# Performance work log

Hardware: AMD Instinct MI355X
Metric: run time of the kernel (lower is better)

Reference implementation:

```python
import jax, jax.numpy as jnp
import numpy as np

B, N, IN_DIM, OUT_DIM, H = 8, 1024, 256, 256, 4
HD = OUT_DIM // H  # head_dim = 64
NEG = -1e9
EPS = 1e-5


def setup_inputs() -> dict:
    key = jax.random.key(0)
    ks = jax.random.split(key, 9)
    h = jax.random.normal(ks[0], (B, N, IN_DIM), dtype=jnp.float32)
    adj = jax.random.randint(ks[1], (N, N), 0, 2, dtype=jnp.int32)
    adj = adj.at[jnp.arange(N), jnp.arange(N)].set(1)  # self loops so no empty rows
    s = 1.0 / np.sqrt(IN_DIM)
    W = jax.random.uniform(ks[2], (H, IN_DIM, HD), jnp.float32, -s, s)
    sa = 1.0 / np.sqrt(2 * HD)
    a1 = jax.random.uniform(ks[3], (H, HD), jnp.float32, -sa, sa)
    a2 = jax.random.uniform(ks[4], (H, HD), jnp.float32, -sa, sa)
    sp = 1.0 / np.sqrt(OUT_DIM)
    proj_w = jax.random.uniform(ks[5], (OUT_DIM, OUT_DIM), jnp.float32, -sp, sp)
    proj_b = jax.random.uniform(ks[6], (OUT_DIM,), jnp.float32, -sp, sp)
    gamma = jnp.ones((OUT_DIM,), jnp.float32)
    beta = jnp.zeros((OUT_DIM,), jnp.float32)
    return {"h": h, "adj": adj, "W": W, "a1": a1, "a2": a2,
            "proj_w": proj_w, "proj_b": proj_b, "gamma": gamma, "beta": beta}


def reference(h, adj, W, a1, a2, proj_w, proj_b, gamma, beta):
    # Wh: [B,H,N,HD]
    Wh = jnp.einsum('bni,hid->bhnd', h, W)
    # Decompose a([Wh_i || Wh_j]) = a1.Wh_i + a2.Wh_j (same math as concat+linear)
    si = jnp.einsum('bhnd,hd->bhn', Wh, a1)  # [B,H,N]
    sj = jnp.einsum('bhnd,hd->bhn', Wh, a2)
    e = jax.nn.leaky_relu(si[:, :, :, None] + sj[:, :, None, :], 0.2)  # [B,H,N,N]
    mask = (adj == 0)  # [N,N]
    e = jnp.where(mask[None, None], NEG, e)
    alpha = jax.nn.softmax(e, axis=-1)
    out = jnp.einsum('bhnm,bhmd->bhnd', alpha, Wh)  # [B,H,N,HD]
    h_multi = out.transpose(0, 2, 1, 3).reshape(B, N, OUT_DIM)  # concat heads
    h_out = jnp.einsum('bnd,od->bno', h_multi, proj_w) + proj_b
    h_out = h_out + h  # residual (in_dim == out_dim)
    mu = jnp.mean(h_out, axis=-1, keepdims=True)
    var = jnp.mean(jnp.square(h_out - mu), axis=-1, keepdims=True)
    return (h_out - mu) * jax.lax.rsqrt(var + EPS) * gamma + beta
```

## Files before the change

### kernel.cpp

```cpp
#include <hip/hip_runtime.h>
#include <hip/hip_bf16.h>

#define NN 1024
#define LOG2E 1.44269504088896f

typedef __attribute__((ext_vector_type(8))) short short8;
typedef __attribute__((ext_vector_type(4))) float floatx4;
typedef __attribute__((ext_vector_type(4))) int intx4;
typedef __attribute__((ext_vector_type(2))) int intx2;

static __device__ __forceinline__ unsigned pk2(float f0, float f1) {
    unsigned u0 = __float_as_uint(f0) + 0x8000u;
    unsigned u1 = __float_as_uint(f1) + 0x8000u;
    return __builtin_amdgcn_perm(u1, u0, 0x07060302u);
}
static __device__ __forceinline__ short8 pk8(floatx4 v0, floatx4 v1) {
    union { intx4 i; short8 s; } u;
    u.i[0] = (int)pk2(v0[0], v0[1]); u.i[1] = (int)pk2(v0[2], v0[3]);
    u.i[2] = (int)pk2(v1[0], v1[1]); u.i[3] = (int)pk2(v1[2], v1[3]);
    return u.s;
}
static __device__ __forceinline__ void load_lds16(const void* gsrc, void* lds) {
    __builtin_amdgcn_global_load_lds(
        (const __attribute__((address_space(1))) void*)gsrc,
        (__attribute__((address_space(3))) void*)lds, 16, 0, 0);
}

__global__ __launch_bounds__(256) void prep_kernel(
    const float* __restrict__ W, const float* __restrict__ proj_w,
    const int* __restrict__ adj,
    __hip_bfloat16* __restrict__ WTb,
    __hip_bfloat16* __restrict__ pwb,
    unsigned* __restrict__ adjT)
{
    int blk = blockIdx.x, t = threadIdx.x;
    if (blk < 16) {
        int o = blk * 16 + (t >> 4);
        int hh = o >> 6, d = o & 63;
        #pragma unroll
        for (int kk = 0; kk < 16; ++kk) {
            int k = (t & 15) + 16 * kk;
            WTb[(size_t)o * 256 + k] = __float2bfloat16(W[((size_t)hh * 256 + k) * 64 + d]);
        }
    } else if (blk < 32) {
        size_t base = (size_t)(blk - 16) * 4096 + (size_t)t * 16;
        #pragma unroll
        for (int k = 0; k < 16; k += 8) {
            floatx4 v0 = *(const floatx4*)(proj_w + base + k);
            floatx4 v1 = *(const floatx4*)(proj_w + base + k + 4);
            *(short8*)(pwb + base + k) = pk8(v0, v1);
        }
    } else {
        int n = (blk - 32) * 8 + (t >> 5);
        int wd = t & 31;
        const int* arow = adj + (size_t)n * NN + wd * 32;
        unsigned bits = 0;
        #pragma unroll
        for (int j4 = 0; j4 < 8; ++j4) {
            intx4 v = *(const intx4*)(arow + j4 * 4);
            #pragma unroll
            for (int j = 0; j < 4; ++j) if (v[j] != 0) bits |= (1u << (j4 * 4 + j));
        }
        adjT[(size_t)wd * NN + n] = bits;
    }
}

__global__ __launch_bounds__(512) void wh_kernel(
    const float* __restrict__ h,
    const __hip_bfloat16* __restrict__ WTb,
    const float* __restrict__ a1, const float* __restrict__ a2,
    __hip_bfloat16* __restrict__ WhTt,
    float* __restrict__ si, float* __restrict__ sj)
{
    __shared__ __align__(16) __hip_bfloat16 WTbs[8][4096];
    __shared__ float redsi[2][4][4][16];
    __shared__ float redsj[2][4][4][16];

    int t = threadIdx.x;
    int w = t >> 6, l = t & 63;
    int rt = w >> 2, ds = w & 3;
    int rl = l & 15, q = l >> 4;
    int bx = blockIdx.x;
    int bb = bx >> 5, tb = bx & 31;

    short8 af[8];
    const float* Arow = h + ((size_t)bb * 1024 + tb * 32 + rt * 16 + rl) * 256 + q * 8;
    #pragma unroll
    for (int k0 = 0; k0 < 8; ++k0) {
        floatx4 v0 = *(const floatx4*)(Arow + k0 * 32);
        floatx4 v1 = *(const floatx4*)(Arow + k0 * 32 + 4);
        af[k0] = pk8(v0, v1);
    }

    int d = ds * 16 + rl;
    int s = rt * 16 + q * 4;
    size_t toff = (size_t)d * 32 + (((s >> 3) ^ (d & 3)) * 8) + (s & 7);
    int srow_ = l >> 5;

    #pragma unroll
    for (int ph = 0; ph < 2; ++ph) {
        if (ph) __syncthreads();
        #pragma unroll
        for (int k = 0; k < 8; ++k) {
            int row = k * 2 + srow_;
            int g = (l & 31) ^ (row & 7);
            load_lds16(WTb + (size_t)(ph * 128 + w * 16 + row) * 256 + g * 8, &WTbs[w][k * 512]);
        }
        __syncthreads();

        #pragma unroll
        for (int jj = 0; jj < 2; ++jj) {
            int head = ph * 2 + jj;
            int lt = ds + 4 * jj;
            floatx4 acc = {0.f, 0.f, 0.f, 0.f};
            #pragma unroll
            for (int k0 = 0; k0 < 8; ++k0) {
                int p = ((k0 << 2) + q) ^ (rl & 7);
                short8 bf = *(const short8*)(&WTbs[lt][rl * 256 + p * 8]);
                acc = __builtin_amdgcn_mfma_f32_16x16x32_bf16(af[k0], bf, acc, 0, 0, 0);
            }

            intx2 pr;
            pr[0] = (int)pk2(acc[0], acc[1]);
            pr[1] = (int)pk2(acc[2], acc[3]);
            *(intx2*)(WhTt + ((size_t)(bb * 4 + head) * 32 + tb) * 2048 + toff) = pr;

            float av1 = a1[head * 64 + d] * LOG2E;
            float av2 = a2[head * 64 + d] * LOG2E;
            #pragma unroll
            for (int i = 0; i < 4; ++i) {
                float p1 = acc[i] * av1, p2 = acc[i] * av2;
                #pragma unroll
                for (int off = 1; off < 16; off <<= 1) {
                    p1 += __shfl_xor(p1, off, 64);
                    p2 += __shfl_xor(p2, off, 64);
                }
                if (rl == 0) { redsi[rt][ds][head][q * 4 + i] = p1; redsj[rt][ds][head][q * 4 + i] = p2; }
            }
        }
    }
    __syncthreads();

    if (t < 128) {
        int head = t >> 5, u = t & 31, rt2 = u >> 4, row = u & 15;
        si[(size_t)(bb * 4 + head) * NN + tb * 32 + rt2 * 16 + row] =
            redsi[rt2][0][head][row] + redsi[rt2][1][head][row] +
            redsi[rt2][2][head][row] + redsi[rt2][3][head][row];
    } else if (t < 256) {
        int u2 = t - 128;
        int head = u2 >> 5, u = u2 & 31, rt2 = u >> 4, row = u & 15;
        sj[(size_t)(bb * 4 + head) * NN + tb * 32 + rt2 * 16 + row] =
            redsj[rt2][0][head][row] + redsj[rt2][1][head][row] +
            redsj[rt2][2][head][row] + redsj[rt2][3][head][row];
    }
}

__global__ __launch_bounds__(256, 4) void attn_kernel(
    const unsigned* __restrict__ adjT,
    const __hip_bfloat16* __restrict__ WhTt,
    const float* __restrict__ si, const float* __restrict__ sj,
    __hip_bfloat16* __restrict__ hmg)
{
    __shared__ __align__(16) __hip_bfloat16 pl[4][16][72];
    __shared__ float accs[4][64][17];
    __shared__ float lsums[4][16];

    int bx = blockIdx.x, t = threadIdx.x;
    int w = t >> 6, l = t & 63;
    int rl = l & 15, q = l >> 4;
    int head = bx & 3, tile = (bx >> 2) & 63, b = bx >> 8;
    int n0 = tile * 16;
    int bh = b * 4 + head;
    int r = l >> 2, cg = l & 3;
    int nr = n0 + r;

    float sii = si[(size_t)bh * NN + nr];
    const float* sjr = sj + (size_t)bh * NN;
    const __hip_bfloat16* Tbh = WhTt + (size_t)bh * 32 * 2048;

    float lsum = 0.f;
    floatx4 acc[4] = { {0,0,0,0}, {0,0,0,0}, {0,0,0,0}, {0,0,0,0} };

    #pragma unroll 2
    for (int it = 0; it < 4; ++it) {
        int mabs = w * 256 + it * 64;
        int t0 = mabs >> 5;
        short8 bf[8];
        #pragma unroll
        for (int ks = 0; ks < 2; ++ks) {
            #pragma unroll
            for (int dt = 0; dt < 4; ++dt)
                bf[ks * 4 + dt] = *(const short8*)(Tbh + (size_t)(t0 + ks) * 2048
                                    + (dt * 16 + rl) * 32 + ((q ^ (rl & 3)) * 8));
        }
        unsigned wA = adjT[(size_t)t0 * NN + nr];
        unsigned wB = adjT[(size_t)(t0 + 1) * NN + nr];
        unsigned half = (cg < 2 ? wA : wB) >> ((cg & 1) * 16);
        int mb = mabs + cg * 16;
        #pragma unroll
        for (int c4 = 0; c4 < 4; ++c4) {
            floatx4 s4 = *(const floatx4*)(sjr + mb + c4 * 4);
            float pv[4];
            #pragma unroll
            for (int k = 0; k < 4; ++k) {
                float x = sii + s4[k];
                x = fmaxf(x, 0.2f * x);
                x = ((half >> (c4 * 4 + k)) & 1u) ? x : -1e9f;
                pv[k] = exp2f(x);
                lsum += pv[k];
            }
            intx2 two;
            two[0] = (int)pk2(pv[0], pv[1]);
            two[1] = (int)pk2(pv[2], pv[3]);
            *(intx2*)(&pl[w][r][cg * 16 + c4 * 4]) = two;
        }
        #pragma unroll
        for (int ks = 0; ks < 2; ++ks) {
            short8 afr = *(const short8*)(&pl[w][rl][ks * 32 + q * 8]);
            #pragma unroll
            for (int dt = 0; dt < 4; ++dt)
                acc[dt] = __builtin_amdgcn_mfma_f32_16x16x32_bf16(afr, bf[ks * 4 + dt], acc[dt], 0, 0, 0);
        }
    }

    lsum += __shfl_xor(lsum, 1, 64);
    lsum += __shfl_xor(lsum, 2, 64);
    if (cg == 0) lsums[w][r] = lsum;
    #pragma unroll
    for (int dt = 0; dt < 4; ++dt) {
        #pragma unroll
        for (int i = 0; i < 4; ++i)
            accs[w][l][dt * 4 + i] = acc[dt][i];
    }
    __syncthreads();

    #pragma unroll
    for (int i = 0; i < 4; ++i) {
        int row = q * 4 + i;
        float riv = 1.f / (lsums[0][row] + lsums[1][row] + lsums[2][row] + lsums[3][row]);
        float cc = accs[0][l][w * 4 + i] + accs[1][l][w * 4 + i]
                 + accs[2][l][w * 4 + i] + accs[3][l][w * 4 + i];
        unsigned uv = (__float_as_uint(cc * riv) + 0x8000u) >> 16;
        hmg[(size_t)(b * 1024 + n0 + row) * 256 + head * 64 + w * 16 + rl]
            = __ushort_as_bfloat16((unsigned short)uv);
    }
}

__global__ __launch_bounds__(256) void proj_kernel(
    const __hip_bfloat16* __restrict__ hmg,
    const __hip_bfloat16* __restrict__ pwb,
    const float* __restrict__ h,
    const float* __restrict__ proj_b, const float* __restrict__ gamma,
    const float* __restrict__ beta,
    float* __restrict__ out)
{
    __shared__ float red[2][4][16];

    int bx = blockIdx.x, t = threadIdx.x;
    int w = t >> 6, l = t & 63;
    int rl = l & 15, q = l >> 4;
    int r0 = bx * 16;

    short8 paf[8];
    #pragma unroll
    for (int k0 = 0; k0 < 8; ++k0)
        paf[k0] = *(const short8*)(hmg + (size_t)(r0 + rl) * 256 + q * 8 + k0 * 32);

    floatx4 pacc[4];
    #pragma unroll
    for (int j = 0; j < 4; ++j) {
        int ct = w + 4 * j;
        const __hip_bfloat16* Bp = pwb + (size_t)(ct * 16 + rl) * 256 + q * 8;
        floatx4 a = {0.f, 0.f, 0.f, 0.f};
        #pragma unroll
        for (int k0 = 0; k0 < 8; ++k0) {
            short8 bfp = *(const short8*)(Bp + k0 * 32);
            a = __builtin_amdgcn_mfma_f32_16x16x32_bf16(paf[k0], bfp, a, 0, 0, 0);
        }
        pacc[j] = a;
    }

    float ps[4] = {0.f, 0.f, 0.f, 0.f};
    #pragma unroll
    for (int j = 0; j < 4; ++j) {
        int col = (w + j * 4) * 16 + rl;
        float pb = proj_b[col];
        #pragma unroll
        for (int i = 0; i < 4; ++i) {
            float v = pacc[j][i] + pb + h[(size_t)(r0 + q * 4 + i) * 256 + col];
            pacc[j][i] = v;
            ps[i] += v;
        }
    }
    #pragma unroll
    for (int i = 0; i < 4; ++i) {
        float s = ps[i];
        #pragma unroll
        for (int off = 1; off < 16; off <<= 1) s += __shfl_xor(s, off, 64);
        ps[i] = s;
    }
    if (rl == 0) {
        for (int i = 0; i < 4; ++i) red[0][w][q * 4 + i] = ps[i];
    }
    __syncthreads();
    float mu[4];
    #pragma unroll
    for (int i = 0; i < 4; ++i) {
        int row = q * 4 + i;
        mu[i] = (red[0][0][row] + red[0][1][row] + red[0][2][row] + red[0][3][row]) * (1.f / 256.f);
    }
    float vs[4] = {0.f, 0.f, 0.f, 0.f};
    #pragma unroll
    for (int j = 0; j < 4; ++j) {
        #pragma unroll
        for (int i = 0; i < 4; ++i) { float cv = pacc[j][i] - mu[i]; vs[i] += cv * cv; }
    }
    #pragma unroll
    for (int i = 0; i < 4; ++i) {
        float s = vs[i];
        #pragma unroll
        for (int off = 1; off < 16; off <<= 1) s += __shfl_xor(s, off, 64);
        vs[i] = s;
    }
    if (rl == 0) {
        for (int i = 0; i < 4; ++i) red[1][w][q * 4 + i] = vs[i];
    }
    __syncthreads();
    float rs[4];
    #pragma unroll
    for (int i = 0; i < 4; ++i) {
        int row = q * 4 + i;
        float var = (red[1][0][row] + red[1][1][row] + red[1][2][row] + red[1][3][row]) * (1.f / 256.f);
        rs[i] = rsqrtf(var + 1e-5f);
    }
    #pragma unroll
    for (int j = 0; j < 4; ++j) {
        int col = (w + j * 4) * 16 + rl;
        float g = gamma[col], be = beta[col];
        #pragma unroll
        for (int i = 0; i < 4; ++i)
            out[(size_t)(r0 + q * 4 + i) * 256 + col] = (pacc[j][i] - mu[i]) * rs[i] * g + be;
    }
}

extern "C" void kernel_launch(void* const* d_in, const int* in_sizes, int n_in,
                              void* d_out, int out_size, void* d_ws, size_t ws_size,
                              hipStream_t stream) {
    const float* h      = (const float*)d_in[0];
    const int*   adj    = (const int*)d_in[1];
    const float* W      = (const float*)d_in[2];
    const float* a1     = (const float*)d_in[3];
    const float* a2     = (const float*)d_in[4];
    const float* proj_w = (const float*)d_in[5];
    const float* proj_b = (const float*)d_in[6];
    const float* gamma  = (const float*)d_in[7];
    const float* beta   = (const float*)d_in[8];
    float* out = (float*)d_out;

    char* ws = (char*)d_ws;
    __hip_bfloat16* WhTt = (__hip_bfloat16*)ws;  ws += (size_t)32 * 32 * 2048 * 2;
    __hip_bfloat16* WTb = (__hip_bfloat16*)ws;   ws += 256 * 256 * 2;
    __hip_bfloat16* pwb = (__hip_bfloat16*)ws;   ws += 256 * 256 * 2;
    float* si = (float*)ws;                      ws += (size_t)32 * NN * 4;
    float* sj = (float*)ws;                      ws += (size_t)32 * NN * 4;
    unsigned* adjT = (unsigned*)ws;              ws += (size_t)NN * 32 * 4;
    __hip_bfloat16* hmg = (__hip_bfloat16*)ws;   ws += (size_t)8 * NN * 256 * 2;

    prep_kernel<<<160, 256, 0, stream>>>(W, proj_w, adj, WTb, pwb, adjT);
    wh_kernel<<<256, 512, 0, stream>>>(h, WTb, a1, a2, WhTt, si, sj);
    attn_kernel<<<2048, 256, 0, stream>>>(adjT, WhTt, si, sj, hmg);
    proj_kernel<<<512, 256, 0, stream>>>(hmg, pwb, h, proj_b, gamma, beta, out);
}
```

Before: 125.4 us.

## Share staged Wh tiles across waves via triple-buffered LDS async loads

The attention kernel now gives each block 64 query rows, with each wave owning 16 rows and sweeping all 1024 keys. Previously a block held 16 rows and split the keys across waves, then reduced through shared memory. Each 64-key tile of Wh^T is loaded once into a triple-buffered LDS ring with global_load_lds and read by all four waves, with manual vmcnt waits and barriers overlapping the next tile's load with the current compute. This removes redundant per-wave global B-fragment loads and the cross-wave accumulator reduction. In exchange the grid drops from 2048 to 512 blocks, and each iteration adds a barrier.

```diff
diff --git a/kernel.cpp b/kernel.cpp
--- a/kernel.cpp
+++ b/kernel.cpp
@@ -8,6 +8,10 @@
 typedef __attribute__((ext_vector_type(4))) float floatx4;
 typedef __attribute__((ext_vector_type(4))) int intx4;
 typedef __attribute__((ext_vector_type(2))) int intx2;
+
+#define WAIT_VM0()   asm volatile("s_waitcnt vmcnt(0)" ::: "memory")
+#define WAIT_VM2()   asm volatile("s_waitcnt vmcnt(2)" ::: "memory")
+#define SCHED_FENCE() asm volatile("" ::: "memory")
 
 static __device__ __forceinline__ unsigned pk2(float f0, float f1) {
     unsigned u0 = __float_as_uint(f0) + 0x8000u;
@@ -161,18 +165,17 @@
     const float* __restrict__ si, const float* __restrict__ sj,
     __hip_bfloat16* __restrict__ hmg)
 {
+    __shared__ __align__(16) __hip_bfloat16 bst[3][4096];
     __shared__ __align__(16) __hip_bfloat16 pl[4][16][72];
-    __shared__ float accs[4][64][17];
-    __shared__ float lsums[4][16];
 
     int bx = blockIdx.x, t = threadIdx.x;
     int w = t >> 6, l = t & 63;
     int rl = l & 15, q = l >> 4;
-    int head = bx & 3, tile = (bx >> 2) & 63, b = bx >> 8;
-    int n0 = tile * 16;
+    int head = bx & 3, qt = (bx >> 2) & 15, b = bx >> 6;
+    int n0 = qt * 64;
     int bh = b * 4 + head;
     int r = l >> 2, cg = l & 3;
-    int nr = n0 + r;
+    int nr = n0 + w * 16 + r;
 
     float sii = si[(size_t)bh * NN + nr];
     const float* sjr = sj + (size_t)bh * NN;
@@ -181,29 +184,33 @@
     float lsum = 0.f;
     floatx4 acc[4] = { {0,0,0,0}, {0,0,0,0}, {0,0,0,0}, {0,0,0,0} };
 
-    #pragma unroll 2
-    for (int it = 0; it < 4; ++it) {
-        int mabs = w * 256 + it * 64;
-        int t0 = mabs >> 5;
-        short8 bf[8];
-        #pragma unroll
-        for (int ks = 0; ks < 2; ++ks) {
-            #pragma unroll
-            for (int dt = 0; dt < 4; ++dt)
-                bf[ks * 4 + dt] = *(const short8*)(Tbh + (size_t)(t0 + ks) * 2048
-                                    + (dt * 16 + rl) * 32 + ((q ^ (rl & 3)) * 8));
-        }
-        unsigned wA = adjT[(size_t)t0 * NN + nr];
-        unsigned wB = adjT[(size_t)(t0 + 1) * NN + nr];
+    #pragma unroll
+    for (int k = 0; k < 2; ++k)
+        load_lds16(Tbh + (w * 2 + k) * 512 + l * 8, &bst[0][(w * 2 + k) * 512]);
+
+    int rb = 0, sb = 1;
+    for (int it = 0; it < 16; ++it) {
+        int mb = it * 64 + cg * 16;
+        floatx4 s4v[4];
+        #pragma unroll
+        for (int c4 = 0; c4 < 4; ++c4) s4v[c4] = *(const floatx4*)(sjr + mb + c4 * 4);
+        unsigned wA = adjT[(size_t)(2 * it) * NN + nr];
+        unsigned wB = adjT[(size_t)(2 * it + 1) * NN + nr];
+        SCHED_FENCE();
+        if (it < 15) {
+            #pragma unroll
+            for (int k = 0; k < 2; ++k)
+                load_lds16(Tbh + (size_t)(it + 1) * 4096 + (w * 2 + k) * 512 + l * 8,
+                           &bst[sb][(w * 2 + k) * 512]);
+        }
+        SCHED_FENCE();
         unsigned half = (cg < 2 ? wA : wB) >> ((cg & 1) * 16);
-        int mb = mabs + cg * 16;
         #pragma unroll
         for (int c4 = 0; c4 < 4; ++c4) {
-            floatx4 s4 = *(const floatx4*)(sjr + mb + c4 * 4);
             float pv[4];
             #pragma unroll
             for (int k = 0; k < 4; ++k) {
-                float x = sii + s4[k];
+                float x = sii + s4v[c4][k];
                 x = fmaxf(x, 0.2f * x);
                 x = ((half >> (c4 * 4 + k)) & 1u) ? x : -1e9f;
                 pv[k] = exp2f(x);
@@ -214,35 +221,32 @@
             two[1] = (int)pk2(pv[2], pv[3]);
             *(intx2*)(&pl[w][r][cg * 16 + c4 * 4]) = two;
         }
+        if (it < 15) { WAIT_VM2(); } else { WAIT_VM0(); }
+        __builtin_amdgcn_s_barrier();
         #pragma unroll
         for (int ks = 0; ks < 2; ++ks) {
             short8 afr = *(const short8*)(&pl[w][rl][ks * 32 + q * 8]);
             #pragma unroll
-            for (int dt = 0; dt < 4; ++dt)
-                acc[dt] = __builtin_amdgcn_mfma_f32_16x16x32_bf16(afr, bf[ks * 4 + dt], acc[dt], 0, 0, 0);
-        }
+            for (int dt = 0; dt < 4; ++dt) {
+                short8 bfr = *(const short8*)(&bst[rb][ks * 2048 + (dt * 16 + rl) * 32 + ((q ^ (rl & 3)) * 8)]);
+                acc[dt] = __builtin_amdgcn_mfma_f32_16x16x32_bf16(afr, bfr, acc[dt], 0, 0, 0);
+            }
+        }
+        rb = sb; sb = (sb == 2) ? 0 : sb + 1;
     }
 
     lsum += __shfl_xor(lsum, 1, 64);
     lsum += __shfl_xor(lsum, 2, 64);
-    if (cg == 0) lsums[w][r] = lsum;
-    #pragma unroll
-    for (int dt = 0; dt < 4; ++dt) {
-        #pragma unroll
-        for (int i = 0; i < 4; ++i)
-            accs[w][l][dt * 4 + i] = acc[dt][i];
-    }
-    __syncthreads();
-
-    #pragma unroll
-    for (int i = 0; i < 4; ++i) {
-        int row = q * 4 + i;
-        float riv = 1.f / (lsums[0][row] + lsums[1][row] + lsums[2][row] + lsums[3][row]);
-        float cc = accs[0][l][w * 4 + i] + accs[1][l][w * 4 + i]
-                 + accs[2][l][w * 4 + i] + accs[3][l][w * 4 + i];
-        unsigned uv = (__float_as_uint(cc * riv) + 0x8000u) >> 16;
-        hmg[(size_t)(b * 1024 + n0 + row) * 256 + head * 64 + w * 16 + rl]
-            = __ushort_as_bfloat16((unsigned short)uv);
+    #pragma unroll
+    for (int i = 0; i < 4; ++i) {
+        float riv = 1.f / __shfl(lsum, (q * 4 + i) * 4, 64);
+        int row = n0 + w * 16 + q * 4 + i;
+        #pragma unroll
+        for (int dt = 0; dt < 4; ++dt) {
+            unsigned uv = (__float_as_uint(acc[dt][i] * riv) + 0x8000u) >> 16;
+            hmg[(size_t)(b * 1024 + row) * 256 + head * 64 + dt * 16 + rl]
+                = __ushort_as_bfloat16((unsigned short)uv);
+        }
     }
 }
 
@@ -368,6 +372,6 @@
 
     prep_kernel<<<160, 256, 0, stream>>>(W, proj_w, adj, WTb, pwb, adjT);
     wh_kernel<<<256, 512, 0, stream>>>(h, WTb, a1, a2, WhTt, si, sj);
-    attn_kernel<<<2048, 256, 0, stream>>>(adjT, WhTt, si, sj, hmg);
+    attn_kernel<<<512, 256, 0, stream>>>(adjT, WhTt, si, sj, hmg);
     proj_kernel<<<512, 256, 0, stream>>>(hmg, pwb, h, proj_b, gamma, beta, out);
 }
```

New measurement: 128.9 us. 1.03x slower.
